# Kernel tuning notes

Measured on AMD Instinct MI355X. Metric: run time of the kernel, lower is better.

## Reference

```python
import jax, jax.numpy as jnp
import numpy as np

EPS = 1e-5


def setup_inputs() -> dict:
    key = jax.random.key(0)
    k1, k2 = jax.random.split(key, 2)
    B, L, C = 2, 385, 128  # L = N+1 tokens (CLS at index 0), N = 384
    x = jax.random.normal(k1, (B, L, C), dtype=jnp.float32)
    gamma = jnp.ones((1, 1, 1, 2 * C), dtype=jnp.float32)
    beta = jnp.zeros((1, 1, 1, 2 * C), dtype=jnp.float32)
    W = jax.random.normal(k2, (C, 2 * C), dtype=jnp.float32) / np.float32(np.sqrt(2 * C))
    b = jnp.zeros((C,), dtype=jnp.float32)
    return {"x": x, "gamma": gamma, "beta": beta, "W": W, "b": b}


def reference(x, gamma, beta, W, b):
    cls_tok = x[:, :1, :]                 # [B,1,C]
    F = x[:, 1:, :]                       # [B,N,C]
    # diff[b,i,j,:] = F[b,j] - F[b,i]  (center i on axis 1, neighbor j on axis 2)
    diff = F[:, None, :, :] - F[:, :, None, :]            # [B,N,N,C]
    var = jnp.var(diff, axis=2, keepdims=True)            # biased var over neighbors, [B,N,1,C]
    F_tilde = diff / jnp.sqrt(var + EPS)                  # [B,N,N,C]
    F_center = jnp.broadcast_to(F[:, :, None, :], diff.shape)
    Fc_K = jnp.concatenate([F_tilde, F_center], axis=-1) * gamma + beta  # [B,N,N,2C]
    weights = jax.nn.softmax(Fc_K, axis=2)                # softmax over neighbors
    Fc_C = jnp.sum(weights * Fc_K, axis=2)                # [B,N,2C]
    tokens = Fc_C @ W.T + b                               # align: Linear(2C -> C)
    return jnp.concatenate([cls_tok, tokens], axis=1)     # [B,L,C]
```

## Files before the change

kernel.cpp:

```cpp
#include <hip/hip_runtime.h>
#include <hip/hip_bf16.h>
#include <math.h>


#define B_  2
#define L_  385
#define C_  128
#define N_  384
#define LC_ (L_ * C_)
#define EPS_ 1e-5f
#define MROWS_ 32
#define RB_  (N_ / MROWS_)
#define LOG2E_ 1.44269504088896340736f

typedef short short8 __attribute__((ext_vector_type(8)));
typedef float f32x4 __attribute__((ext_vector_type(4)));

union V16 { ushort us[8]; uint4 v4; };
union U16 { uint4 v4; short8 s8; };

__device__ inline ushort f2bf(float f) {
  __hip_bfloat16 hb = __float2bfloat16(f);
  return __builtin_bit_cast(ushort, hb);
}

__device__ inline float fast_exp2(float xv) {
#if __has_builtin(__builtin_amdgcn_exp2f)
  return __builtin_amdgcn_exp2f(xv);
#else
  float r;
  asm("v_exp_f32 %0, %1" : "=v"(r) : "v"(xv));
  return r;
#endif
}

__global__ __launch_bounds__(1024, 1) void lnp_prep(
    const float* __restrict__ x, const float* __restrict__ gamma,
    const float* __restrict__ beta, const float* __restrict__ W,
    float* __restrict__ wsNegS, float* __restrict__ wsFac,
    ushort* __restrict__ wsWbf, float* __restrict__ out) {
  const int blk = blockIdx.x;
  const int t   = threadIdx.x;

  if (blk >= 2) {
    const int base = (blk - 2) * 8192 + t * 8;
    const float4 wa  = *(const float4*)&W[base];
    const float4 wb2 = *(const float4*)&W[base + 4];
    V16 pk;
    pk.us[0] = f2bf(wa.x);  pk.us[1] = f2bf(wa.y);
    pk.us[2] = f2bf(wa.z);  pk.us[3] = f2bf(wa.w);
    pk.us[4] = f2bf(wb2.x); pk.us[5] = f2bf(wb2.y);
    pk.us[6] = f2bf(wb2.z); pk.us[7] = f2bf(wb2.w);
    *(uint4*)&wsWbf[base] = pk.v4;
    if (blk == 2 && t < C_) out[t] = x[t];
    if (blk == 3 && t < C_) out[LC_ + t] = x[LC_ + t];
    return;
  }

  __shared__ __align__(16) float p1[16][128], p2[16][128];
  __shared__ float sA[128], slA[128], shA[128];

  const int b  = blk;
  const float* Fb = x + (size_t)b * LC_ + C_;
  const int tc = t & 31;
  const int c4 = tc * 4;
  const int h  = t >> 5;
  const int w  = t >> 6;
  const int l  = t & 63;

  float4 v[12];
  {
    const float* p = Fb + (size_t)(h * 12) * C_ + c4;
#pragma unroll
    for (int r = 0; r < 12; ++r)
      v[r] = *(const float4*)(p + (size_t)r * C_);

    float ax = 0.f, ay = 0.f, az = 0.f, aw = 0.f;
    float qx = 0.f, qy = 0.f, qz = 0.f, qw = 0.f;
#pragma unroll
    for (int r = 0; r < 12; ++r) {
      ax += v[r].x; qx = fmaf(v[r].x, v[r].x, qx);
      ay += v[r].y; qy = fmaf(v[r].y, v[r].y, qy);
      az += v[r].z; qz = fmaf(v[r].z, v[r].z, qz);
      aw += v[r].w; qw = fmaf(v[r].w, v[r].w, qw);
    }
    ax += __shfl_xor(ax, 32); ay += __shfl_xor(ay, 32);
    az += __shfl_xor(az, 32); aw += __shfl_xor(aw, 32);
    qx += __shfl_xor(qx, 32); qy += __shfl_xor(qy, 32);
    qz += __shfl_xor(qz, 32); qw += __shfl_xor(qw, 32);
    if (l < 32) {
      float4 s1 = {ax, ay, az, aw};
      float4 s2 = {qx, qy, qz, qw};
      *(float4*)&p1[w][c4] = s1;
      *(float4*)&p2[w][c4] = s2;
    }
  }
  __syncthreads();

  if (t < 128) {
    float s1 = 0.f, s2 = 0.f;
#pragma unroll
    for (int g = 0; g < 16; ++g) { s1 += p1[g][t]; s2 += p2[g][t]; }
    const float mean = s1 * (1.0f / N_);
    const float var  = fmaxf(s2 * (1.0f / N_) - mean * mean, 0.0f);
    const float s    = gamma[t] * rsqrtf(var + EPS_);
    const float sl   = s * LOG2E_;
    sA[t] = s; slA[t] = sl; shA[t] = sl * mean;
    wsNegS[b * 128 + t] = -s;
  }
  __syncthreads();

  {
    const float4 sl4 = *(const float4*)&slA[c4];
    const float4 sh4 = *(const float4*)&shA[c4];
    float ex = 0.f, ey = 0.f, ez = 0.f, ew = 0.f;
    float fx = 0.f, fy = 0.f, fz = 0.f, fw = 0.f;
#pragma unroll
    for (int r = 0; r < 12; ++r) {
      const float e0 = fast_exp2(fmaf(sl4.x, v[r].x, -sh4.x));
      const float e1 = fast_exp2(fmaf(sl4.y, v[r].y, -sh4.y));
      const float e2 = fast_exp2(fmaf(sl4.z, v[r].z, -sh4.z));
      const float e3 = fast_exp2(fmaf(sl4.w, v[r].w, -sh4.w));
      ex += e0; fx = fmaf(e0, v[r].x, fx);
      ey += e1; fy = fmaf(e1, v[r].y, fy);
      ez += e2; fz = fmaf(e2, v[r].z, fz);
      ew += e3; fw = fmaf(e3, v[r].w, fw);
    }
    ex += __shfl_xor(ex, 32); ey += __shfl_xor(ey, 32);
    ez += __shfl_xor(ez, 32); ew += __shfl_xor(ew, 32);
    fx += __shfl_xor(fx, 32); fy += __shfl_xor(fy, 32);
    fz += __shfl_xor(fz, 32); fw += __shfl_xor(fw, 32);
    if (l < 32) {
      float4 se = {ex, ey, ez, ew};
      float4 sf = {fx, fy, fz, fw};
      *(float4*)&p1[w][c4] = se;
      *(float4*)&p2[w][c4] = sf;
    }
  }
  __syncthreads();

  if (t < 128) {
    float se = 0.f, sf = 0.f;
#pragma unroll
    for (int g = 0; g < 16; ++g) { se += p1[g][t]; sf += p2[g][t]; }
    wsFac[b * 128 + t] = fmaf(sA[t], sf / se, beta[t]);
  }
}

__global__ __launch_bounds__(1024, 1) void lnp_main(
    const float* __restrict__ x, const float* __restrict__ gamma,
    const float* __restrict__ beta, const float* __restrict__ bvec,
    const float* __restrict__ wsNegS, const float* __restrict__ wsFac,
    const ushort* __restrict__ wsWbf, float* __restrict__ out) {
  __shared__ __align__(16) ushort As[MROWS_ * 256];

  const int blk = blockIdx.x;
  const int b   = blk / RB_;
  const int rt  = blk % RB_;
  const int r0  = rt * MROWS_;
  const int t   = threadIdx.x;
  const int wv  = t >> 6;
  const int l   = t & 63;
  const int l16 = l & 15;
  const int lg  = l >> 4;
  const int tn  = wv & 7;
  const int tm  = wv >> 3;
  const int bc  = tn * 16 + l16;
  const int ar  = tm * 16 + l16;

  const int ai  = t >> 5;
  const int kk0 = (t & 31) * 8;
  const int ks  = kk0 & 127;
  const float* fp = x + (size_t)b * LC_ + C_ + (size_t)(r0 + ai) * C_ + ks;
  const float4 af0 = *(const float4*)fp;
  const float4 af1 = *(const float4*)(fp + 4);
  const float* pA = (kk0 < 128) ? (wsNegS + b * 128 + kk0) : (gamma + kk0);
  const float* pB = (kk0 < 128) ? (wsFac + b * 128 + kk0) : (beta + kk0);
  const float4 cA0 = *(const float4*)pA;
  const float4 cA1 = *(const float4*)(pA + 4);
  const float4 cB0 = *(const float4*)pB;
  const float4 cB1 = *(const float4*)(pB + 4);

  U16 wb[8];
  const ushort* wrow = wsWbf + bc * 256 + lg * 8;
#pragma unroll
  for (int kt = 0; kt < 8; ++kt)
    wb[kt].v4 = *(const uint4*)(wrow + kt * 32);
  const float bb = bvec[bc];

  {
    V16 pk;
    pk.us[0] = f2bf(fmaf(cA0.x, af0.x, cB0.x));
    pk.us[1] = f2bf(fmaf(cA0.y, af0.y, cB0.y));
    pk.us[2] = f2bf(fmaf(cA0.z, af0.z, cB0.z));
    pk.us[3] = f2bf(fmaf(cA0.w, af0.w, cB0.w));
    pk.us[4] = f2bf(fmaf(cA1.x, af1.x, cB1.x));
    pk.us[5] = f2bf(fmaf(cA1.y, af1.y, cB1.y));
    pk.us[6] = f2bf(fmaf(cA1.z, af1.z, cB1.z));
    pk.us[7] = f2bf(fmaf(cA1.w, af1.w, cB1.w));
    *(uint4*)&As[ai * 256 + (kk0 ^ ((ai & 7) << 3))] = pk.v4;
  }
  __syncthreads();

  {
    const int abase = ar * 256;
    const int aswz  = (ar & 7) << 3;
    f32x4 acc = {0.f, 0.f, 0.f, 0.f};
#pragma unroll
    for (int kt = 0; kt < 8; ++kt) {
      const int kk = kt * 32 + lg * 8;
      const short8 av = *(const short8*)&As[abase + (kk ^ aswz)];
      acc = __builtin_amdgcn_mfma_f32_16x16x32_bf16(av, wb[kt].s8, acc, 0, 0, 0);
    }
    float* ob = out + (size_t)b * LC_;
#pragma unroll
    for (int r = 0; r < 4; ++r) {
      const int m = tm * 16 + lg * 4 + r;
      ob[(size_t)(1 + r0 + m) * C_ + bc] = acc[r] + bb;
    }
  }
}

extern "C" void kernel_launch(void* const* d_in, const int* in_sizes, int n_in,
                              void* d_out, int out_size, void* d_ws, size_t ws_size,
                              hipStream_t stream) {
  const float* x     = (const float*)d_in[0];
  const float* gamma = (const float*)d_in[1];
  const float* beta  = (const float*)d_in[2];
  const float* W     = (const float*)d_in[3];
  const float* bvec  = (const float*)d_in[4];
  float* out = (float*)d_out;

  float*  wsNegS = (float*)d_ws;
  float*  wsFac  = wsNegS + 256;
  ushort* wsWbf  = (ushort*)(wsNegS + 512);

  lnp_prep<<<6, 1024, 0, stream>>>(x, gamma, beta, W, wsNegS, wsFac, wsWbf, out);
  lnp_main<<<B_ * RB_, 1024, 0, stream>>>(x, gamma, beta, bvec,
                                          wsNegS, wsFac, wsWbf, out);
}
```

Measured before the change: 15.83 us.

## Fuse prep and GEMM kernels into one launch with redundant per-block statistics

```diff
diff --git a/kernel.cpp b/kernel.cpp
--- a/kernel.cpp
+++ b/kernel.cpp
@@ -11,13 +11,13 @@
 #define EPS_ 1e-5f
 #define MROWS_ 32
 #define RB_  (N_ / MROWS_)
+#define NTHR_ 1024
 #define LOG2E_ 1.44269504088896340736f
 
 typedef short short8 __attribute__((ext_vector_type(8)));
 typedef float f32x4 __attribute__((ext_vector_type(4)));
 
 union V16 { ushort us[8]; uint4 v4; };
-union U16 { uint4 v4; short8 s8; };
 
 __device__ inline ushort f2bf(float f) {
   __hip_bfloat16 hb = __float2bfloat16(f);
@@ -34,47 +34,76 @@
 #endif
 }
 
-__global__ __launch_bounds__(1024, 1) void lnp_prep(
+__global__ __launch_bounds__(NTHR_, 1) void lnp_kernel(
     const float* __restrict__ x, const float* __restrict__ gamma,
     const float* __restrict__ beta, const float* __restrict__ W,
-    float* __restrict__ wsNegS, float* __restrict__ wsFac,
-    ushort* __restrict__ wsWbf, float* __restrict__ out) {
+    const float* __restrict__ bvec, float* __restrict__ out) {
+  __shared__ __align__(16) float p1[16][128], p2[16][128];
+  __shared__ __align__(16) float slA[128], shA[128];
+  __shared__ __align__(16) float coefA[256], coefB[256];
+  __shared__ __align__(16) ushort Wb[128 * 256];
+  __shared__ __align__(16) ushort As[MROWS_ * 256];
+
   const int blk = blockIdx.x;
+  const int b   = blk / RB_;
+  const int rt  = blk % RB_;
+  const int r0  = rt * MROWS_;
   const int t   = threadIdx.x;
-
-  if (blk >= 2) {
-    const int base = (blk - 2) * 8192 + t * 8;
-    const float4 wa  = *(const float4*)&W[base];
-    const float4 wb2 = *(const float4*)&W[base + 4];
-    V16 pk;
-    pk.us[0] = f2bf(wa.x);  pk.us[1] = f2bf(wa.y);
-    pk.us[2] = f2bf(wa.z);  pk.us[3] = f2bf(wa.w);
-    pk.us[4] = f2bf(wb2.x); pk.us[5] = f2bf(wb2.y);
-    pk.us[6] = f2bf(wb2.z); pk.us[7] = f2bf(wb2.w);
-    *(uint4*)&wsWbf[base] = pk.v4;
-    if (blk == 2 && t < C_) out[t] = x[t];
-    if (blk == 3 && t < C_) out[LC_ + t] = x[LC_ + t];
-    return;
-  }
-
-  __shared__ __align__(16) float p1[16][128], p2[16][128];
-  __shared__ float sA[128], slA[128], shA[128];
-
-  const int b  = blk;
+  const int l   = t & 63;
+  const int w   = t >> 6;
+
   const float* Fb = x + (size_t)b * LC_ + C_;
-  const int tc = t & 31;
-  const int c4 = tc * 4;
+
+  const int l16 = l & 15;
+  const int lg  = l >> 4;
+  const int tn  = w & 7;
+  const int tm  = w >> 3;
+  const int bc  = tn * 16 + l16;
+  const int ar  = tm * 16 + l16;
+
+  const int c4 = (t & 31) * 4;
   const int h  = t >> 5;
-  const int w  = t >> 6;
-  const int l  = t & 63;
-
   float4 v[12];
   {
     const float* p = Fb + (size_t)(h * 12) * C_ + c4;
 #pragma unroll
     for (int r = 0; r < 12; ++r)
       v[r] = *(const float4*)(p + (size_t)r * C_);
-
+  }
+  const int ai  = t >> 5;
+  const int kk0 = (t & 31) * 8;
+  const int ks  = kk0 & 127;
+  float4 af0, af1;
+  {
+    const float* fp = Fb + (size_t)(r0 + ai) * C_ + ks;
+    af0 = *(const float4*)fp;
+    af1 = *(const float4*)(fp + 4);
+  }
+  const int cW  = t >> 3;
+  const int kb  = (t & 7) * 32;
+  const int swzW = (cW & 7) << 3;
+  float4 wv[8];
+  {
+    const float* wp = &W[cW * 256 + kb];
+#pragma unroll
+    for (int q = 0; q < 8; ++q) wv[q] = *(const float4*)(wp + q * 4);
+  }
+  const float bb = bvec[bc];
+
+  if (rt == 0 && t < C_)
+    out[(size_t)b * LC_ + t] = x[(size_t)b * LC_ + t];
+
+#pragma unroll
+  for (int q = 0; q < 4; ++q) {
+    V16 pk;
+    pk.us[0] = f2bf(wv[2 * q].x);     pk.us[1] = f2bf(wv[2 * q].y);
+    pk.us[2] = f2bf(wv[2 * q].z);     pk.us[3] = f2bf(wv[2 * q].w);
+    pk.us[4] = f2bf(wv[2 * q + 1].x); pk.us[5] = f2bf(wv[2 * q + 1].y);
+    pk.us[6] = f2bf(wv[2 * q + 1].z); pk.us[7] = f2bf(wv[2 * q + 1].w);
+    *(uint4*)&Wb[cW * 256 + ((kb + q * 8) ^ swzW)] = pk.v4;
+  }
+
+  {
     float ax = 0.f, ay = 0.f, az = 0.f, aw = 0.f;
     float qx = 0.f, qy = 0.f, qz = 0.f, qw = 0.f;
 #pragma unroll
@@ -105,8 +134,10 @@
     const float var  = fmaxf(s2 * (1.0f / N_) - mean * mean, 0.0f);
     const float s    = gamma[t] * rsqrtf(var + EPS_);
     const float sl   = s * LOG2E_;
-    sA[t] = s; slA[t] = sl; shA[t] = sl * mean;
-    wsNegS[b * 128 + t] = -s;
+    slA[t] = sl; shA[t] = sl * mean;
+    coefA[t]       = -s;
+    coefA[128 + t] = gamma[128 + t];
+    coefB[128 + t] = beta[128 + t];
   }
   __syncthreads();
 
@@ -143,52 +174,15 @@
     float se = 0.f, sf = 0.f;
 #pragma unroll
     for (int g = 0; g < 16; ++g) { se += p1[g][t]; sf += p2[g][t]; }
-    wsFac[b * 128 + t] = fmaf(sA[t], sf / se, beta[t]);
-  }
-}
-
-__global__ __launch_bounds__(1024, 1) void lnp_main(
-    const float* __restrict__ x, const float* __restrict__ gamma,
-    const float* __restrict__ beta, const float* __restrict__ bvec,
-    const float* __restrict__ wsNegS, const float* __restrict__ wsFac,
-    const ushort* __restrict__ wsWbf, float* __restrict__ out) {
-  __shared__ __align__(16) ushort As[MROWS_ * 256];
-
-  const int blk = blockIdx.x;
-  const int b   = blk / RB_;
-  const int rt  = blk % RB_;
-  const int r0  = rt * MROWS_;
-  const int t   = threadIdx.x;
-  const int wv  = t >> 6;
-  const int l   = t & 63;
-  const int l16 = l & 15;
-  const int lg  = l >> 4;
-  const int tn  = wv & 7;
-  const int tm  = wv >> 3;
-  const int bc  = tn * 16 + l16;
-  const int ar  = tm * 16 + l16;
-
-  const int ai  = t >> 5;
-  const int kk0 = (t & 31) * 8;
-  const int ks  = kk0 & 127;
-  const float* fp = x + (size_t)b * LC_ + C_ + (size_t)(r0 + ai) * C_ + ks;
-  const float4 af0 = *(const float4*)fp;
-  const float4 af1 = *(const float4*)(fp + 4);
-  const float* pA = (kk0 < 128) ? (wsNegS + b * 128 + kk0) : (gamma + kk0);
-  const float* pB = (kk0 < 128) ? (wsFac + b * 128 + kk0) : (beta + kk0);
-  const float4 cA0 = *(const float4*)pA;
-  const float4 cA1 = *(const float4*)(pA + 4);
-  const float4 cB0 = *(const float4*)pB;
-  const float4 cB1 = *(const float4*)(pB + 4);
-
-  U16 wb[8];
-  const ushort* wrow = wsWbf + bc * 256 + lg * 8;
-#pragma unroll
-  for (int kt = 0; kt < 8; ++kt)
-    wb[kt].v4 = *(const uint4*)(wrow + kt * 32);
-  const float bb = bvec[bc];
-
-  {
+    coefB[t] = fmaf(-coefA[t], sf / se, beta[t]);
+  }
+  __syncthreads();
+
+  {
+    const float4 cA0 = *(const float4*)&coefA[kk0];
+    const float4 cA1 = *(const float4*)&coefA[kk0 + 4];
+    const float4 cB0 = *(const float4*)&coefB[kk0];
+    const float4 cB1 = *(const float4*)&coefB[kk0 + 4];
     V16 pk;
     pk.us[0] = f2bf(fmaf(cA0.x, af0.x, cB0.x));
     pk.us[1] = f2bf(fmaf(cA0.y, af0.y, cB0.y));
@@ -205,12 +199,15 @@
   {
     const int abase = ar * 256;
     const int aswz  = (ar & 7) << 3;
+    const int bbase = bc * 256;
+    const int bswz  = (bc & 7) << 3;
     f32x4 acc = {0.f, 0.f, 0.f, 0.f};
 #pragma unroll
     for (int kt = 0; kt < 8; ++kt) {
       const int kk = kt * 32 + lg * 8;
       const short8 av = *(const short8*)&As[abase + (kk ^ aswz)];
-      acc = __builtin_amdgcn_mfma_f32_16x16x32_bf16(av, wb[kt].s8, acc, 0, 0, 0);
+      const short8 bv = *(const short8*)&Wb[bbase + (kk ^ bswz)];
+      acc = __builtin_amdgcn_mfma_f32_16x16x32_bf16(av, bv, acc, 0, 0, 0);
     }
     float* ob = out + (size_t)b * LC_;
 #pragma unroll
@@ -231,11 +228,5 @@
   const float* bvec  = (const float*)d_in[4];
   float* out = (float*)d_out;
 
-  float*  wsNegS = (float*)d_ws;
-  float*  wsFac  = wsNegS + 256;
-  ushort* wsWbf  = (ushort*)(wsNegS + 512);
-
-  lnp_prep<<<6, 1024, 0, stream>>>(x, gamma, beta, W, wsNegS, wsFac, wsWbf, out);
-  lnp_main<<<B_ * RB_, 1024, 0, stream>>>(x, gamma, beta, bvec,
-                                          wsNegS, wsFac, wsWbf, out);
-}
+  lnp_kernel<<<B_ * RB_, NTHR_, 0, stream>>>(x, gamma, beta, W, bvec, out);
+}
```

Measured after the change: 15.10 us. 4.6% less time.
